# Kernel optimization log

Measured on AMD Instinct MI355X. Metric: run time of the kernel, lower is better.

## Reference

```python
import jax, jax.numpy as jnp
import numpy as np

EPS = 1e-5  # torch F.instance_norm default eps

def _inorm(x):
    # instance norm over the flattened spatial axis, per (batch, channel)
    m = jnp.mean(x, axis=-1, keepdims=True)
    v = jnp.var(x, axis=-1, keepdims=True)  # biased variance, matches torch
    return (x - m) / jnp.sqrt(v + EPS)

def _conv1x1(x, w, b):
    # x: (b, c, n), w: (o, c), b: (o,) -- Conv1d with kernel_size=1
    return jnp.einsum('bcn,oc->bon', x, w) + b[None, :, None]

def setup_inputs() -> dict:
    key = jax.random.key(0)
    ks = jax.random.split(key, 8)
    B, C, N, M = 4, 256, 4096, 4096
    sc = 1.0 / np.sqrt(C)  # kaiming-ish fan-in scale for 1x1 conv
    return {
        'q': jax.random.normal(ks[0], (B, C, N), jnp.float32),
        'k': jax.random.normal(ks[1], (B, C, M), jnp.float32),
        'w_q': jax.random.normal(ks[2], (C, C), jnp.float32) * sc,
        'b_q': jnp.zeros((C,), jnp.float32),
        'w_k': jax.random.normal(ks[3], (C, C), jnp.float32) * sc,
        'b_k': jnp.zeros((C,), jnp.float32),
        'w_s': jax.random.normal(ks[4], (C, C), jnp.float32) * sc,
        'b_s': jnp.zeros((C,), jnp.float32),
    }

def reference(q, k, w_q, b_q, w_k, b_k, w_s, b_s):
    # c = q, s = k (module aliases them)
    qe = _conv1x1(_inorm(q), w_q, b_q).transpose(0, 2, 1)   # (b, N, C)
    ke = _conv1x1(_inorm(k), w_k, b_k)                      # (b, C, M)
    se = _conv1x1(k, w_s, b_s).transpose(0, 2, 1)           # (b, M, C)
    attn = jax.nn.softmax(jnp.einsum('bnc,bcm->bnm', qe, ke), axis=-1)  # (b, N, M)
    mean = jnp.einsum('bnm,bmc->bnc', attn, se)             # attn-weighted mean
    var = jax.nn.relu(jnp.einsum('bnm,bmc->bnc', attn, se * se) - mean * mean)
    std = jnp.sqrt(var)
    cs = _inorm(q) * std.transpose(0, 2, 1) + mean.transpose(0, 2, 1)  # (b, C, N)
    return cs
```

## Files before the change

kernel.cpp:

```cpp
#include <hip/hip_runtime.h>
#include <hip/hip_bf16.h>
#include <cstdint>

typedef unsigned short u16;
typedef __attribute__((ext_vector_type(8))) _Float16 half8;
typedef __attribute__((ext_vector_type(2))) __fp16 fp16x2;
typedef __attribute__((ext_vector_type(4))) float f32x4;

#define B_ 4
#define C_ 256
#define N_ 4096
#define M_ 4096
#define QB 32
#define KVB 32
#define LOG2E 1.44269504088896340736f

__device__ __forceinline__ u16 f2h(float x){
  _Float16 h = (_Float16)x;
  return __builtin_bit_cast(u16, h);
}
__device__ __forceinline__ float h2f(u16 h){
  return (float)__builtin_bit_cast(_Float16, h);
}
__device__ __forceinline__ unsigned pkrtz(float a, float b){
  fp16x2 h = __builtin_amdgcn_cvt_pkrtz(a, b);
  return __builtin_bit_cast(unsigned, h);
}
__device__ __forceinline__ float sum2(unsigned w){
  fp16x2 h = __builtin_bit_cast(fp16x2, w);
  return (float)h.x + (float)h.y;
}
__device__ __forceinline__ void gll16(const void* gsrc, void* ldst){
  __builtin_amdgcn_global_load_lds(
      (const __attribute__((address_space(1))) unsigned int*)gsrc,
      (__attribute__((address_space(3))) unsigned int*)ldst, 16, 0, 0);
}
__device__ __forceinline__ void bar_lds(){
  asm volatile("s_waitcnt lgkmcnt(0)" ::: "memory");
  __builtin_amdgcn_s_barrier();
}

__global__ __launch_bounds__(256) void k_stats(const float* __restrict__ q,
                                               const float* __restrict__ k,
                                               float* __restrict__ sq,
                                               float* __restrict__ sk){
  int row = blockIdx.x;
  const float* src = (row < 1024) ? (q + (size_t)row * N_)
                                  : (k + (size_t)(row - 1024) * N_);
  float s = 0.f, ss = 0.f;
  for (int i = threadIdx.x; i < N_/4; i += 256){
    float4 v = ((const float4*)src)[i];
    s  += v.x + v.y + v.z + v.w;
    ss += v.x*v.x + v.y*v.y + v.z*v.z + v.w*v.w;
  }
  #pragma unroll
  for (int off = 32; off >= 1; off >>= 1){
    s  += __shfl_down(s, off);
    ss += __shfl_down(ss, off);
  }
  __shared__ float rs[4], rss[4];
  int w = threadIdx.x >> 6;
  if ((threadIdx.x & 63) == 0){ rs[w] = s; rss[w] = ss; }
  __syncthreads();
  if (threadIdx.x == 0){
    s  = rs[0]+rs[1]+rs[2]+rs[3];
    ss = rss[0]+rss[1]+rss[2]+rss[3];
    float m   = s * (1.f/N_);
    float var = ss * (1.f/N_) - m*m;
    float r   = rsqrtf(fmaxf(var, 0.f) + 1e-5f);
    float* dst = (row < 1024) ? (sq + row*2) : (sk + (row-1024)*2);
    dst[0] = m; dst[1] = r;
  }
}

__global__ __launch_bounds__(64) void k_wprep(
    const float* __restrict__ wq, const float* __restrict__ bq,
    const float* __restrict__ wk, const float* __restrict__ bk,
    const float* __restrict__ wsw, const float* __restrict__ bs,
    const float* __restrict__ sq, const float* __restrict__ sk,
    u16* __restrict__ wh, u16* __restrict__ wl, float* __restrict__ bias2)
{
  int co = blockIdx.x, z = blockIdx.y;
  int lane = threadIdx.x;
  const float* W; const float* bias; const float* st = nullptr; float sc = 1.f;
  if (z < 4){ W = wq; bias = bq; st = sq + z*512; sc = LOG2E; }
  else if (z < 8){ W = wk; bias = bk; st = sk + (z-4)*512; }
  else { W = wsw; bias = bs; }
  float4 wv = *(const float4*)(W + co*256 + lane*4);
  float w4[4] = {wv.x, wv.y, wv.z, wv.w};
  float vs[4];
  float bsum = 0.f;
  if (st){
    float4 s0 = *(const float4*)(st + lane*8);
    float4 s1 = *(const float4*)(st + lane*8 + 4);
    float mm[4] = {s0.x, s0.z, s1.x, s1.z};
    float rr[4] = {s0.y, s0.w, s1.y, s1.w};
    #pragma unroll
    for (int i=0;i<4;i++){
      vs[i] = w4[i]*rr[i]*sc;
      bsum += w4[i]*rr[i]*mm[i];
    }
  } else {
    #pragma unroll
    for (int i=0;i<4;i++) vs[i] = w4[i];
  }
  u16 hi[4], lo[4];
  #pragma unroll
  for (int i=0;i<4;i++){
    hi[i] = f2h(vs[i]);
    lo[i] = f2h(vs[i] - h2f(hi[i]));
  }
  size_t idx = ((size_t)(z*8 + (lane>>3))*256 + co)*32 + ((lane>>1)&3)*8 + (lane&1)*4;
  *(uint2*)(wh + idx) = make_uint2((unsigned)hi[0] | ((unsigned)hi[1]<<16),
                                   (unsigned)hi[2] | ((unsigned)hi[3]<<16));
  *(uint2*)(wl + idx) = make_uint2((unsigned)lo[0] | ((unsigned)lo[1]<<16),
                                   (unsigned)lo[2] | ((unsigned)lo[3]<<16));
  #pragma unroll
  for (int off = 32; off >= 1; off >>= 1) bsum += __shfl_down(bsum, off);
  if (lane == 0) bias2[z*256 + co] = sc*(bias[co] - bsum);
}

__global__ __launch_bounds__(256, 3) void k_conv(
    const float* __restrict__ q, const float* __restrict__ kk,
    const u16* __restrict__ wh, const u16* __restrict__ wl,
    const float* __restrict__ bias2,
    u16* __restrict__ qe, u16* __restrict__ kt, u16* __restrict__ se)
{
  __shared__ u16 XT[64*256];
  const int tid = threadIdx.x;
  const int spt = blockIdx.x, bz = blockIdx.y;
  const int b = bz / 3, mode = bz - b*3;
  const int sp0 = spt*64;
  const float* X = (mode==0 ? q : kk) + (size_t)b*C_*N_;
  const int z = (mode==0) ? b : (mode==1 ? 4+b : 8);
  const u16* whp = wh + (size_t)z*8*256*32;
  const u16* wlp = wl + (size_t)z*8*256*32;
  const float* bp = bias2 + z*256;

  {
    int kc_l = tid & 15, spq = tid >> 4;
    #pragma unroll
    for (int i=0;i<16;i++){
      int kc = i*16 + kc_l;
      float4 v = *(const float4*)(X + (size_t)kc*N_ + sp0 + spq*4);
      float vv[4] = {v.x, v.y, v.z, v.w};
      #pragma unroll
      for (int e=0;e<4;e++){
        int sp = spq*4 + e;
        int byte = sp*512 + (((kc>>3) ^ (sp&7)) << 4) + (kc&7)*2;
        *(u16*)((char*)XT + byte) = f2h(vv[e]);
      }
    }
  }
  __syncthreads();

  const int wid = tid>>6, lane = tid&63, l15 = lane&15, lg = lane>>4;
  f32x4 acc[4][4];
  #pragma unroll
  for (int i=0;i<4;i++)
    #pragma unroll
    for (int j=0;j<4;j++) acc[i][j] = (f32x4)(0.f);

  #pragma unroll
  for (int ks=0; ks<8; ++ks){
    half8 xf[4];
    #pragma unroll
    for (int st=0; st<4; ++st)
      xf[st] = *(const half8*)((char*)XT + (st*16 + l15)*512 + (((ks*4+lg) ^ (l15&7)) << 4));
    #pragma unroll
    for (int ct=0; ct<4; ++ct){
      size_t woff = ((size_t)(ks*256 + wid*64 + ct*16 + l15))*32 + lg*8;
      half8 bh = *(const half8*)(whp + woff);
      half8 bl = *(const half8*)(wlp + woff);
      #pragma unroll
      for (int st=0; st<4; ++st){
        if (mode < 2){
          acc[st][ct] = __builtin_amdgcn_mfma_f32_16x16x32_f16(xf[st], bh, acc[st][ct], 0,0,0);
          acc[st][ct] = __builtin_amdgcn_mfma_f32_16x16x32_f16(xf[st], bl, acc[st][ct], 0,0,0);
        } else {
          acc[ct][st] = __builtin_amdgcn_mfma_f32_16x16x32_f16(bh, xf[st], acc[ct][st], 0,0,0);
          acc[ct][st] = __builtin_amdgcn_mfma_f32_16x16x32_f16(bl, xf[st], acc[ct][st], 0,0,0);
        }
      }
    }
  }

  if (mode < 2){
    u16* o = (mode==0 ? qe : kt);
    #pragma unroll
    for (int st=0; st<4; ++st){
      #pragma unroll
      for (int ct=0; ct<4; ++ct){
        int co = wid*64 + ct*16 + l15;
        float bb = bp[co];
        #pragma unroll
        for (int r=0;r<4;r++){
          int sp = sp0 + st*16 + lg*4 + r;
          o[(size_t)(b*N_ + sp)*C_ + co] = f2h(acc[st][ct][r] + bb);
        }
      }
    }
  } else {
    #pragma unroll
    for (int ct=0; ct<4; ++ct){
      #pragma unroll
      for (int st=0; st<4; ++st){
        #pragma unroll
        for (int r=0;r<4;r++){
          int co = wid*64 + ct*16 + lg*4 + r;
          float bb = bp[co];
          se[(size_t)(b*C_ + co)*M_ + sp0 + st*16 + l15] = f2h(acc[ct][st][r] + bb);
        }
      }
    }
  }
}

__global__ __launch_bounds__(256, 2) void k_attn(
    const float* __restrict__ q, const float* __restrict__ stq,
    const u16* __restrict__ qe_g, const u16* __restrict__ kt_g,
    const u16* __restrict__ se_g, float* __restrict__ out)
{
  __shared__ u16 KTs[2][KVB*256];
  __shared__ u16 SEs[2][C_*KVB];
  __shared__ unsigned WTw[QB*16];
  __shared__ float PMX[4][16];
  __shared__ float SRES[QB];
  __shared__ float LRUNS[2][QB];
  __shared__ int FLG[2];

  const int tid = threadIdx.x;
  const int wid = tid >> 6, lane = tid & 63;
  const int l15 = lane & 15, lg = lane >> 4;
  const int qg = wid & 1, mh = wid >> 1;
  const int b = blockIdx.y;
  const int n0 = blockIdx.x * QB;

  half8 qf[8];
  {
    const u16* qb = qe_g + ((size_t)(b*N_ + n0 + qg*16 + l15))*C_;
    #pragma unroll
    for (int ks=0; ks<8; ++ks) qf[ks] = *(const half8*)(qb + ks*32 + lg*8);
  }

  int ktsrc[4], sesrc[4];
  #pragma unroll
  for (int i=0;i<4;i++){
    int g = (i*4 + wid)*64 + lane;
    int row = g >> 5, cin = g & 31;
    ktsrc[i] = row*512 + ((cin ^ (row & 7)) << 4);
    int c = g >> 2, mch = (g & 3) ^ ((c >> 1) & 3);
    sesrc[i] = c*8192 + mch*16;
  }
  const char* ktg = (const char*)kt_g + (size_t)b*M_*512;
  const char* seg = (const char*)se_g + (size_t)b*C_*M_*2;

  float m_run = -1e30f, lrun = 0.f;
  f32x4 accm[2][4], accs[2][4];
  #pragma unroll
  for (int i=0;i<2;i++)
    #pragma unroll
    for (int j=0;j<4;j++){ accm[i][j] = (f32x4)(0.f); accs[i][j] = (f32x4)(0.f); }

  #pragma unroll
  for (int i=0;i<4;i++){
    int o = (i*4 + wid)*1024;
    gll16(ktg + ktsrc[i], (char*)&KTs[0][0] + o);
    gll16(seg + sesrc[i], (char*)&SEs[0][0] + o);
  }

  for (int t=0; t<M_/KVB; ++t){
    const int buf = t & 1;
    __syncthreads();

    if (t+1 < M_/KVB){
      const int nb = buf ^ 1;
      int koff = (t+1)*(KVB*512);
      int soff = (t+1)*(KVB*2);
      #pragma unroll
      for (int i=0;i<4;i++){
        int o = (i*4 + wid)*1024;
        gll16(ktg + koff + ktsrc[i], (char*)&KTs[nb][0] + o);
        gll16(seg + soff + sesrc[i], (char*)&SEs[nb][0] + o);
      }
    }

    f32x4 L0 = (f32x4)(0.f);
    {
      const char* ktb = (const char*)&KTs[buf][0];
      int krow = mh*16 + l15;
      #pragma unroll
      for (int ks=0; ks<8; ++ks){
        half8 a0 = *(const half8*)(ktb + krow*512 + (((ks*4 + lg) ^ (l15 & 7)) << 4));
        L0 = __builtin_amdgcn_mfma_f32_16x16x32_f16(a0, qf[ks], L0, 0,0,0);
      }
    }
    float pm = fmaxf(fmaxf(L0[0], L0[1]), fmaxf(L0[2], L0[3]));
    pm = fmaxf(pm, __shfl_xor(pm, 16));
    pm = fmaxf(pm, __shfl_xor(pm, 32));
    if (lg == 0) PMX[wid][l15] = pm;
    bar_lds();

    float m_tile = fmaxf(pm, PMX[wid ^ 2][l15]);
    int flag = __any(m_tile > m_run + 8.0f);
    float sv = 1.0f;
    if (flag){
      float mn = fmaxf(m_run, m_tile);
      sv = exp2f(m_run - mn);
      m_run = mn;
    }
    if (mh == 0 && lg == 0) SRES[qg*16 + l15] = sv;
    if (mh == 0 && lane == 0) FLG[qg] = flag;
    unsigned W0 = pkrtz(exp2f(L0[0]-m_run), exp2f(L0[1]-m_run));
    unsigned W1 = pkrtz(exp2f(L0[2]-m_run), exp2f(L0[3]-m_run));
    {
      int row = qg*16 + l15;
      int c16 = (mh*2 + (lg >> 1)) ^ ((l15 >> 1) & 3);
      *(uint2*)((char*)WTw + row*64 + (c16 << 4) + ((lg & 1) << 3)) = make_uint2(W0, W1);
    }
    float rs = sum2(W0) + sum2(W1);
    rs += __shfl_xor(rs, 16);
    rs += __shfl_xor(rs, 32);
    lrun = lrun * sv + rs;
    bar_lds();

    if (FLG[0] | FLG[1]){
      #pragma unroll
      for (int rt=0;rt<2;rt++){
        f32x4 s4 = *(const f32x4*)&SRES[rt*16 + lg*4];
        #pragma unroll
        for (int ct=0;ct<4;ct++){
          #pragma unroll
          for (int r=0;r<4;r++){ accm[rt][ct][r] *= s4[r]; accs[rt][ct][r] *= s4[r]; }
        }
      }
    }

    {
      half8 a[2];
      #pragma unroll
      for (int rt=0;rt<2;rt++){
        int row = rt*16 + l15;
        a[rt] = *(const half8*)((char*)WTw + row*64 + ((lg ^ ((l15>>1)&3)) << 4));
      }
      const char* seb = (const char*)&SEs[buf][0];
      #pragma unroll
      for (int ct=0;ct<4;ct++){
        int c = wid*64 + ct*16 + l15;
        half8 v = *(const half8*)(seb + c*64 + ((lg ^ ((c>>1)&3)) << 4));
        half8 h2 = v * v;
        half8 l2;
#if __has_builtin(__builtin_elementwise_fma)
        l2 = __builtin_elementwise_fma(v, v, -h2);
#else
        #pragma unroll
        for (int e=0;e<8;e++){ float vf=(float)v[e]; l2[e]=(_Float16)(vf*vf-(float)h2[e]); }
#endif
        #pragma unroll
        for (int rt=0;rt<2;rt++){
          accm[rt][ct] = __builtin_amdgcn_mfma_f32_16x16x32_f16(a[rt], v,  accm[rt][ct], 0,0,0);
          accs[rt][ct] = __builtin_amdgcn_mfma_f32_16x16x32_f16(a[rt], h2, accs[rt][ct], 0,0,0);
          accs[rt][ct] = __builtin_amdgcn_mfma_f32_16x16x32_f16(a[rt], l2, accs[rt][ct], 0,0,0);
        }
      }
    }
  }

  if (lg == 0) LRUNS[mh][qg*16 + l15] = lrun;
  __syncthreads();

  #pragma unroll
  for (int rt=0;rt<2;rt++){
    f32x4 lv0 = *(const f32x4*)&LRUNS[0][rt*16 + lg*4];
    f32x4 lv1 = *(const f32x4*)&LRUNS[1][rt*16 + lg*4];
    f32x4 inv;
    #pragma unroll
    for (int r=0;r<4;r++) inv[r] = 1.f / (lv0[r] + lv1[r]);
    #pragma unroll
    for (int ct=0;ct<4;ct++){
      int c = wid*64 + ct*16 + l15;
      float2 st = *(const float2*)(stq + (size_t)(b*C_ + c)*2);
      size_t base = ((size_t)(b*C_ + c))*(size_t)N_ + (size_t)(n0 + rt*16 + lg*4);
      f32x4 qv = *(const f32x4*)(q + base);
      f32x4 res;
      #pragma unroll
      for (int r=0;r<4;r++){
        float mean = accm[rt][ct][r] * inv[r];
        float ms   = accs[rt][ct][r] * inv[r];
        float sd   = sqrtf(fmaxf(ms - mean*mean, 0.f));
        float qn   = (qv[r] - st.x) * st.y;
        res[r] = qn * sd + mean;
      }
      *(f32x4*)(out + base) = res;
    }
  }
}

extern "C" void kernel_launch(void* const* d_in, const int* in_sizes, int n_in,
                              void* d_out, int out_size, void* d_ws, size_t ws_size,
                              hipStream_t stream){
  const float* q   = (const float*)d_in[0];
  const float* k   = (const float*)d_in[1];
  const float* wq  = (const float*)d_in[2];
  const float* bq  = (const float*)d_in[3];
  const float* wk  = (const float*)d_in[4];
  const float* bk  = (const float*)d_in[5];
  const float* wsw = (const float*)d_in[6];
  const float* bs  = (const float*)d_in[7];
  float* out = (float*)d_out;

  char* w = (char*)d_ws;
  float* stq = (float*)w;
  float* stk = (float*)(w + 8192);
  u16* wh    = (u16*)(w + 16384);
  u16* wl    = (u16*)(w + 16384 + 1179648);
  float* bias2 = (float*)(w + 16384 + 2*1179648);
  char* big  = w + 16384 + 2*1179648 + 16384;
  u16* qe  = (u16*)big;
  u16* kt  = qe + (size_t)B_*N_*C_;
  u16* se  = kt + (size_t)B_*M_*C_;

  k_stats<<<dim3(2048), dim3(256), 0, stream>>>(q, k, stq, stk);
  k_wprep<<<dim3(256, 9), dim3(64), 0, stream>>>(wq, bq, wk, bk, wsw, bs,
                                                 stq, stk, wh, wl, bias2);
  k_conv<<<dim3(64, 12), dim3(256), 0, stream>>>(q, k, wh, wl, bias2, qe, kt, se);
  k_attn<<<dim3(N_/QB, B_), dim3(256), 0, stream>>>(q, stq, qe, kt, se, out);
}
```

Baseline: 252.5 us.

## Single-buffer SE tile in LDS, raise occupancy to three blocks, add MFMA priority

Result: slower. 282.7 us (+12.0%).

```diff
diff --git a/kernel.cpp b/kernel.cpp
--- a/kernel.cpp
+++ b/kernel.cpp
@@ -6,6 +6,7 @@
 typedef __attribute__((ext_vector_type(8))) _Float16 half8;
 typedef __attribute__((ext_vector_type(2))) __fp16 fp16x2;
 typedef __attribute__((ext_vector_type(4))) float f32x4;
+typedef __attribute__((ext_vector_type(4))) unsigned u32x4;
 
 #define B_ 4
 #define C_ 256
@@ -13,6 +14,7 @@
 #define M_ 4096
 #define QB 32
 #define KVB 32
+#define NT (M_/KVB)
 #define LOG2E 1.44269504088896340736f
 
 __device__ __forceinline__ u16 f2h(float x){
@@ -38,6 +40,20 @@
 __device__ __forceinline__ void bar_lds(){
   asm volatile("s_waitcnt lgkmcnt(0)" ::: "memory");
   __builtin_amdgcn_s_barrier();
+}
+__device__ __forceinline__ void sq_hl(half8 v, half8& h2, half8& l2){
+  u32x4 vw = __builtin_bit_cast(u32x4, v);
+  u32x4 hw, lw;
+  #pragma unroll
+  for (int j=0;j<4;j++){
+    unsigned h, l;
+    asm("v_pk_mul_f16 %0, %1, %1" : "=v"(h) : "v"(vw[j]));
+    asm("v_pk_fma_f16 %0, %1, %1, %2 neg_lo:[0,0,1] neg_hi:[0,0,1]"
+        : "=v"(l) : "v"(vw[j]), "v"(h));
+    hw[j] = h; lw[j] = l;
+  }
+  h2 = __builtin_bit_cast(half8, hw);
+  l2 = __builtin_bit_cast(half8, lw);
 }
 
 __global__ __launch_bounds__(256) void k_stats(const float* __restrict__ q,
@@ -216,13 +232,13 @@
   }
 }
 
-__global__ __launch_bounds__(256, 2) void k_attn(
+__global__ __launch_bounds__(256, 3) void k_attn(
     const float* __restrict__ q, const float* __restrict__ stq,
     const u16* __restrict__ qe_g, const u16* __restrict__ kt_g,
     const u16* __restrict__ se_g, float* __restrict__ out)
 {
   __shared__ u16 KTs[2][KVB*256];
-  __shared__ u16 SEs[2][C_*KVB];
+  __shared__ u16 SEL[C_*KVB];
   __shared__ unsigned WTw[QB*16];
   __shared__ float PMX[4][16];
   __shared__ float SRES[QB];
@@ -263,37 +279,38 @@
     for (int j=0;j<4;j++){ accm[i][j] = (f32x4)(0.f); accs[i][j] = (f32x4)(0.f); }
 
   #pragma unroll
-  for (int i=0;i<4;i++){
-    int o = (i*4 + wid)*1024;
-    gll16(ktg + ktsrc[i], (char*)&KTs[0][0] + o);
-    gll16(seg + sesrc[i], (char*)&SEs[0][0] + o);
-  }
-
-  for (int t=0; t<M_/KVB; ++t){
+  for (int i=0;i<4;i++)
+    gll16(ktg + ktsrc[i], (char*)&KTs[0][0] + (i*4 + wid)*1024);
+
+  for (int t=0; t<NT; ++t){
     const int buf = t & 1;
     __syncthreads();
 
-    if (t+1 < M_/KVB){
-      const int nb = buf ^ 1;
-      int koff = (t+1)*(KVB*512);
-      int soff = (t+1)*(KVB*2);
-      #pragma unroll
-      for (int i=0;i<4;i++){
-        int o = (i*4 + wid)*1024;
-        gll16(ktg + koff + ktsrc[i], (char*)&KTs[nb][0] + o);
-        gll16(seg + soff + sesrc[i], (char*)&SEs[nb][0] + o);
-      }
+    {
+      int soff = t*(KVB*2);
+      #pragma unroll
+      for (int i=0;i<4;i++)
+        gll16(seg + soff + sesrc[i], (char*)&SEL[0] + (i*4 + wid)*1024);
+    }
+    {
+      int tn = (t+1 == NT) ? 0 : t+1;
+      int koff = tn*(KVB*512);
+      #pragma unroll
+      for (int i=0;i<4;i++)
+        gll16(ktg + koff + ktsrc[i], (char*)&KTs[buf^1][0] + (i*4 + wid)*1024);
     }
 
     f32x4 L0 = (f32x4)(0.f);
     {
       const char* ktb = (const char*)&KTs[buf][0];
       int krow = mh*16 + l15;
+      __builtin_amdgcn_s_setprio(1);
       #pragma unroll
       for (int ks=0; ks<8; ++ks){
         half8 a0 = *(const half8*)(ktb + krow*512 + (((ks*4 + lg) ^ (l15 & 7)) << 4));
         L0 = __builtin_amdgcn_mfma_f32_16x16x32_f16(a0, qf[ks], L0, 0,0,0);
       }
+      __builtin_amdgcn_s_setprio(0);
     }
     float pm = fmaxf(fmaxf(L0[0], L0[1]), fmaxf(L0[2], L0[3]));
     pm = fmaxf(pm, __shfl_xor(pm, 16));
@@ -322,6 +339,8 @@
     rs += __shfl_xor(rs, 16);
     rs += __shfl_xor(rs, 32);
     lrun = lrun * sv + rs;
+
+    asm volatile("s_waitcnt vmcnt(4)" ::: "memory");
     bar_lds();
 
     if (FLG[0] | FLG[1]){
@@ -343,25 +362,21 @@
         int row = rt*16 + l15;
         a[rt] = *(const half8*)((char*)WTw + row*64 + ((lg ^ ((l15>>1)&3)) << 4));
       }
-      const char* seb = (const char*)&SEs[buf][0];
+      const char* seb = (const char*)&SEL[0];
       #pragma unroll
       for (int ct=0;ct<4;ct++){
         int c = wid*64 + ct*16 + l15;
         half8 v = *(const half8*)(seb + c*64 + ((lg ^ ((c>>1)&3)) << 4));
-        half8 h2 = v * v;
-        half8 l2;
-#if __has_builtin(__builtin_elementwise_fma)
-        l2 = __builtin_elementwise_fma(v, v, -h2);
-#else
-        #pragma unroll
-        for (int e=0;e<8;e++){ float vf=(float)v[e]; l2[e]=(_Float16)(vf*vf-(float)h2[e]); }
-#endif
+        half8 h2, l2;
+        sq_hl(v, h2, l2);
+        __builtin_amdgcn_s_setprio(1);
         #pragma unroll
         for (int rt=0;rt<2;rt++){
           accm[rt][ct] = __builtin_amdgcn_mfma_f32_16x16x32_f16(a[rt], v,  accm[rt][ct], 0,0,0);
           accs[rt][ct] = __builtin_amdgcn_mfma_f32_16x16x32_f16(a[rt], h2, accs[rt][ct], 0,0,0);
           accs[rt][ct] = __builtin_amdgcn_mfma_f32_16x16x32_f16(a[rt], l2, accs[rt][ct], 0,0,0);
         }
+        __builtin_amdgcn_s_setprio(0);
       }
     }
   }
```
